# Kernel optimization log

Hardware: AMD Instinct MI355X
Metric: run time of the kernel (lower is better)

The kernel has to match this reference:

```python
import jax, jax.numpy as jnp
import numpy as np

B, DZ, H, DY = 4096, 512, 2048, 10
N_STEPS = 64
SCALE = 0.02  # matches param_ulow/uhigh magnitude


def setup_inputs() -> dict:
    key = jax.random.key(0)
    ks = jax.random.split(key, 6)
    x = jax.random.normal(ks[0], (B, DZ), dtype=jnp.float32)
    A = jax.random.normal(ks[1], (DZ, DZ), dtype=jnp.float32) * SCALE
    W1 = jax.random.normal(ks[2], (H, DZ), dtype=jnp.float32) * SCALE
    b1 = jax.random.normal(ks[3], (H,), dtype=jnp.float32) * SCALE
    W2 = jax.random.normal(ks[4], (DY, H), dtype=jnp.float32) * SCALE
    b2 = jax.random.normal(ks[5], (DY,), dtype=jnp.float32) * SCALE
    return {"x": x, "A": A, "W1": W1, "b1": b1, "W2": W2, "b2": b2,
            "n_steps": N_STEPS}


def reference(x, A, W1, b1, W2, b2, n_steps):
    # Z0 = P @ x with P = I  => Z0 = x
    # dz/dt = einsum('ji,bi->bj', A, z) = z @ A.T ; explicit Euler on [0, 1]
    dt = jnp.float32(1.0 / n_steps)

    def euler_step(z, _):
        return z + dt * (z @ A.T), None

    zT, _ = jax.lax.scan(euler_step, x, None, length=n_steps)  # [B, DZ]
    # Q MLP (n_layers=3): Linear -> ReLU -> Linear
    h = jax.nn.relu(zT @ W1.T + b1)  # [B, H]
    y = h @ W2.T + b2                # [B, DY]
    return y
```

## Files before the change

kernel.cpp:

```cpp
#include <hip/hip_runtime.h>
#include <hip/hip_bf16.h>

#define B_SZ 4096
#define DZ   512
#define H_SZ 2048
#define DY   10

#define C2 0.4921875f
#define C3 0.158935546875f
#define C4 0.037872314453125f
#define C5 ((float)(7624512.0/1073741824.0))
#define C6 ((float)(74974368.0/68719476736.0))

typedef __attribute__((ext_vector_type(8))) __bf16 bf16x8;
typedef __attribute__((ext_vector_type(4))) float  f32x4;
typedef __attribute__((ext_vector_type(8))) unsigned short us8;

__device__ inline unsigned short f2bf(float f) {
    unsigned u = __float_as_uint(f);
    u += 0x7fffu + ((u >> 16) & 1u);
    return (unsigned short)(u >> 16);
}
__device__ inline float bf2f(unsigned short s) {
    return __uint_as_float(((unsigned)s) << 16);
}

union SqSmem {
    struct { unsigned short A[64 * 64]; unsigned short B[64 * 64]; } s;
    float epi[64 * 68];
};

#define MFMA_STEP(acc)                                                        \
    {                                                                         \
        _Pragma("unroll")                                                     \
        for (int ks = 0; ks < 2; ++ks) {                                      \
            bf16x8 af[2], bfr[2];                                             \
            _Pragma("unroll")                                                 \
            for (int i = 0; i < 2; ++i) {                                     \
                int ra = wm + i * 16 + l16, ca = (ks * 4 + quad) ^ (ra & 7);  \
                af[i] = *(const bf16x8*)&sm.s.A[ra * 64 + ca * 8];            \
                int rb = wn + i * 16 + l16, cb = (ks * 4 + quad) ^ (rb & 7);  \
                bfr[i] = *(const bf16x8*)&sm.s.B[rb * 64 + cb * 8];           \
            }                                                                 \
            _Pragma("unroll")                                                 \
            for (int i = 0; i < 2; ++i)                                       \
                _Pragma("unroll")                                             \
                for (int j = 0; j < 2; ++j)                                   \
                    acc[i][j] = __builtin_amdgcn_mfma_f32_16x16x32_bf16(      \
                        af[i], bfr[j], acc[i][j], 0, 0, 0);                   \
        }                                                                     \
    }

#define ACC_TO_EPI(acc)                                                       \
    {                                                                         \
        _Pragma("unroll")                                                     \
        for (int i = 0; i < 2; ++i)                                           \
            _Pragma("unroll")                                                 \
            for (int j = 0; j < 2; ++j)                                       \
                _Pragma("unroll")                                             \
                for (int rr = 0; rr < 4; ++rr)                                \
                    sm.epi[(wm + i * 16 + quad * 4 + rr) * 68 +               \
                           wn + j * 16 + l16] = acc[i][j][rr];                \
        __syncthreads();                                                      \
    }

__device__ inline void gemm64_mfma(const unsigned short* __restrict__ Arows,
                                   const unsigned short* __restrict__ Brows,
                                   int m0, int n0, int t, SqSmem& sm) {
    const int lane = t & 63, w = t >> 6, quad = lane >> 4, l16 = lane & 15;
    const int wm = (w & 1) * 32, wn = (w >> 1) * 32;
    f32x4 acc[2][2];
#pragma unroll
    for (int i = 0; i < 2; ++i)
#pragma unroll
        for (int j = 0; j < 2; ++j) acc[i][j] = (f32x4){0.f, 0.f, 0.f, 0.f};
    for (int kt = 0; kt < 8; ++kt) {
#pragma unroll
        for (int c = 0; c < 2; ++c) {
            int idx = c * 256 + t, row = idx >> 3, cc = idx & 7;
            int ccs = cc ^ (row & 7);
            *(us8*)&sm.s.A[row * 64 + ccs * 8] =
                *(const us8*)&Arows[(size_t)(m0 + row) * 512 + kt * 64 + cc * 8];
            *(us8*)&sm.s.B[row * 64 + ccs * 8] =
                *(const us8*)&Brows[(size_t)(n0 + row) * 512 + kt * 64 + cc * 8];
        }
        __syncthreads();
        MFMA_STEP(acc)
        __syncthreads();
    }
    ACC_TO_EPI(acc)
}

__device__ inline void gemm64_f32src(const float* __restrict__ Arows,
                                     const float* __restrict__ Bsrc,
                                     int m0, int n0, int t, SqSmem& sm) {
    const int lane = t & 63, w = t >> 6, quad = lane >> 4, l16 = lane & 15;
    const int wm = (w & 1) * 32, wn = (w >> 1) * 32;
    const int r = t >> 2, cq = t & 3;
    f32x4 acc[2][2];
#pragma unroll
    for (int i = 0; i < 2; ++i)
#pragma unroll
        for (int j = 0; j < 2; ++j) acc[i][j] = (f32x4){0.f, 0.f, 0.f, 0.f};
    for (int kt = 0; kt < 8; ++kt) {
        float va[16];
#pragma unroll
        for (int u = 0; u < 4; ++u) {
            float4 f = *(const float4*)&Arows[(size_t)(m0 + r) * 512 + kt * 64 + cq * 16 + u * 4];
            va[u * 4 + 0] = f.x; va[u * 4 + 1] = f.y;
            va[u * 4 + 2] = f.z; va[u * 4 + 3] = f.w;
        }
#pragma unroll
        for (int j2 = 0; j2 < 2; ++j2) {
            us8 h;
#pragma unroll
            for (int j = 0; j < 8; ++j) h[j] = f2bf(va[j2 * 8 + j]);
            int cc = cq * 2 + j2;
            *(us8*)&sm.s.A[r * 64 + (cc ^ (r & 7)) * 8] = h;
        }
#pragma unroll
        for (int u = 0; u < 4; ++u) {
            float4 f = *(const float4*)&Bsrc[(size_t)(kt * 64 + r) * 512 + n0 + cq * 16 + u * 4];
            float vv[4] = {f.x, f.y, f.z, f.w};
#pragma unroll
            for (int j = 0; j < 4; ++j) {
                int n = cq * 16 + u * 4 + j;
                sm.s.B[n * 64 + ((r >> 3) ^ (n & 7)) * 8 + (r & 7)] = f2bf(vv[j]);
            }
        }
        __syncthreads();
        MFMA_STEP(acc)
        __syncthreads();
    }
    ACC_TO_EPI(acc)
}

__device__ inline void epi_out_bf(unsigned short* __restrict__ dst, int m0,
                                  int n0, int t, SqSmem& sm) {
    const int r = t >> 2, cq = t & 3;
    us8 h0, h1;
#pragma unroll
    for (int j = 0; j < 8; ++j) {
        h0[j] = f2bf(sm.epi[r * 68 + cq * 16 + j]);
        h1[j] = f2bf(sm.epi[r * 68 + cq * 16 + 8 + j]);
    }
    *(us8*)&dst[(size_t)(m0 + r) * 512 + n0 + cq * 16]     = h0;
    *(us8*)&dst[(size_t)(m0 + r) * 512 + n0 + cq * 16 + 8] = h1;
}
__device__ inline void epi_out_bfT(unsigned short* __restrict__ dst, int m0,
                                   int n0, int t, SqSmem& sm) {
    const int cf = t >> 2, rq = t & 3;
    us8 o0, o1;
#pragma unroll
    for (int i = 0; i < 8; ++i) {
        o0[i] = f2bf(sm.epi[(rq * 16 + i) * 68 + cf]);
        o1[i] = f2bf(sm.epi[(rq * 16 + 8 + i) * 68 + cf]);
    }
    *(us8*)&dst[(size_t)(n0 + cf) * 512 + m0 + rq * 16]     = o0;
    *(us8*)&dst[(size_t)(n0 + cf) * 512 + m0 + rq * 16 + 8] = o1;
}

__global__ __launch_bounds__(256) void k_s1(
    const float* __restrict__ A, const float* __restrict__ x,
    const float* __restrict__ W1, const float* __restrict__ b2,
    unsigned short* __restrict__ A2_bf, unsigned short* __restrict__ A2T_bf,
    unsigned short* __restrict__ AT_bf, unsigned short* __restrict__ U1_bf,
    unsigned short* __restrict__ x_bf, float* __restrict__ y) {
    __shared__ SqSmem sm;
    const int b = blockIdx.x, t = threadIdx.x;
    const int gid = b * 256 + t;

    const float4* x4 = (const float4*)x;
#pragma unroll
    for (int i = 0; i < 3; ++i) {
        int id = gid + i * 98304;
        if (id < 262144) {
            float4 v0 = x4[(size_t)id * 2], v1 = x4[(size_t)id * 2 + 1];
            us8 o;
            o[0] = f2bf(v0.x); o[1] = f2bf(v0.y); o[2] = f2bf(v0.z); o[3] = f2bf(v0.w);
            o[4] = f2bf(v1.x); o[5] = f2bf(v1.y); o[6] = f2bf(v1.z); o[7] = f2bf(v1.w);
            *(us8*)&x_bf[(size_t)id * 8] = o;
        }
    }
    if (gid < B_SZ * DY) y[gid] = b2[gid % 10];

    if (b < 64) {
        const int m0 = (b >> 3) * 64, n0 = (b & 7) * 64;
        gemm64_f32src(A, A, m0, n0, t, sm);
        epi_out_bf(A2_bf, m0, n0, t, sm);
        epi_out_bfT(A2T_bf, m0, n0, t, sm);
    } else if (b < 128) {
        const int bb = b - 64, m0 = (bb >> 3) * 64, n0 = (bb & 7) * 64;
        const int r = t >> 2, cq = t & 3;
#pragma unroll
        for (int u = 0; u < 4; ++u) {
            float4 f = *(const float4*)&A[(size_t)(m0 + r) * 512 + n0 + cq * 16 + u * 4];
            sm.epi[r * 68 + cq * 16 + u * 4 + 0] = f.x;
            sm.epi[r * 68 + cq * 16 + u * 4 + 1] = f.y;
            sm.epi[r * 68 + cq * 16 + u * 4 + 2] = f.z;
            sm.epi[r * 68 + cq * 16 + u * 4 + 3] = f.w;
        }
        __syncthreads();
        epi_out_bfT(AT_bf, m0, n0, t, sm);
    } else {
        const int bb = b - 128, m0 = (bb >> 3) * 64, n0 = (bb & 7) * 64;
        gemm64_f32src(W1, A, m0, n0, t, sm);
        epi_out_bf(U1_bf, m0, n0, t, sm);
    }
}

__global__ __launch_bounds__(256) void k_s2(
    const unsigned short* __restrict__ A2_bf,
    const unsigned short* __restrict__ A2T_bf,
    const unsigned short* __restrict__ AT_bf,
    const unsigned short* __restrict__ U1_bf,
    unsigned short* __restrict__ A3T_bf, unsigned short* __restrict__ U2_bf,
    unsigned short* __restrict__ U3_bf) {
    __shared__ SqSmem sm;
    const int b = blockIdx.x, t = threadIdx.x;
    if (b < 64) {
        const int m0 = (b >> 3) * 64, n0 = (b & 7) * 64;
        gemm64_mfma(A2_bf, AT_bf, m0, n0, t, sm);
        epi_out_bfT(A3T_bf, m0, n0, t, sm);
    } else if (b < 320) {
        const int bb = b - 64, m0 = (bb >> 3) * 64, n0 = (bb & 7) * 64;
        gemm64_mfma(U1_bf, AT_bf, m0, n0, t, sm);
        epi_out_bf(U2_bf, m0, n0, t, sm);
    } else {
        const int bb = b - 320, m0 = (bb >> 3) * 64, n0 = (bb & 7) * 64;
        gemm64_mfma(U1_bf, A2T_bf, m0, n0, t, sm);
        epi_out_bf(U3_bf, m0, n0, t, sm);
    }
}

__global__ __launch_bounds__(256) void k_s3(
    const float* __restrict__ W1, const unsigned short* __restrict__ U1_bf,
    const unsigned short* __restrict__ U2_bf,
    const unsigned short* __restrict__ U3_bf,
    const unsigned short* __restrict__ A3T_bf,
    unsigned short* __restrict__ w1f) {
    __shared__ SqSmem sm;
    const int b = blockIdx.x, t = threadIdx.x;
    const int m0 = (b >> 3) * 64, n0 = (b & 7) * 64;
    const int lane = t & 63, w = t >> 6, quad = lane >> 4, l16 = lane & 15;
    const int wm = (w & 1) * 32, wn = (w >> 1) * 32;
    f32x4 acc[2][2];
#pragma unroll
    for (int i = 0; i < 2; ++i)
#pragma unroll
        for (int j = 0; j < 2; ++j) acc[i][j] = (f32x4){0.f, 0.f, 0.f, 0.f};
    for (int kt = 0; kt < 8; ++kt) {
#pragma unroll
        for (int c = 0; c < 2; ++c) {
            int idx = c * 256 + t, row = idx >> 3, cc = idx & 7;
            int ccs = cc ^ (row & 7);
            size_t ga = (size_t)(m0 + row) * 512 + kt * 64 + cc * 8;
            us8 u1 = *(const us8*)&U1_bf[ga];
            us8 u2 = *(const us8*)&U2_bf[ga];
            us8 u3 = *(const us8*)&U3_bf[ga];
            us8 g;
#pragma unroll
            for (int j = 0; j < 8; ++j)
                g[j] = f2bf(C4 * bf2f(u1[j]) + C5 * bf2f(u2[j]) + C6 * bf2f(u3[j]));
            *(us8*)&sm.s.A[row * 64 + ccs * 8] = g;
            *(us8*)&sm.s.B[row * 64 + ccs * 8] =
                *(const us8*)&A3T_bf[(size_t)(n0 + row) * 512 + kt * 64 + cc * 8];
        }
        __syncthreads();
        MFMA_STEP(acc)
        __syncthreads();
    }
    ACC_TO_EPI(acc)
    const int r = t >> 2, cq = t & 3;
    size_t gbase = (size_t)(m0 + r) * 512 + n0 + cq * 16;
    us8 u1a = *(const us8*)&U1_bf[gbase], u1b = *(const us8*)&U1_bf[gbase + 8];
    us8 u2a = *(const us8*)&U2_bf[gbase], u2b = *(const us8*)&U2_bf[gbase + 8];
    us8 u3a = *(const us8*)&U3_bf[gbase], u3b = *(const us8*)&U3_bf[gbase + 8];
    us8 h0, h1;
#pragma unroll
    for (int u = 0; u < 2; ++u) {
        float4 wv = *(const float4*)&W1[gbase + u * 4];
        float4 wv2 = *(const float4*)&W1[gbase + 8 + u * 4];
#pragma unroll
        for (int j = 0; j < 4; ++j) {
            int e = u * 4 + j;
            float wj = (j == 0 ? wv.x : j == 1 ? wv.y : j == 2 ? wv.z : wv.w);
            float wj2 = (j == 0 ? wv2.x : j == 1 ? wv2.y : j == 2 ? wv2.z : wv2.w);
            h0[e] = f2bf(wj + bf2f(u1a[e]) + C2 * bf2f(u2a[e]) +
                         C3 * bf2f(u3a[e]) + sm.epi[r * 68 + cq * 16 + e]);
            h1[e] = f2bf(wj2 + bf2f(u1b[e]) + C2 * bf2f(u2b[e]) +
                         C3 * bf2f(u3b[e]) + sm.epi[r * 68 + cq * 16 + 8 + e]);
        }
    }
    *(us8*)&w1f[gbase]     = h0;
    *(us8*)&w1f[gbase + 8] = h1;
}

union SmemU {
    struct { unsigned short A[128 * 64]; unsigned short B[128 * 64]; } s;
    struct { unsigned short h[128 * 130]; float w2[DY * 132]; } e;
};

__global__ __launch_bounds__(256, 2) void mlp_kernel(
    const unsigned short* __restrict__ x_bf,
    const unsigned short* __restrict__ w1f,
    const float* __restrict__ b1, const float* __restrict__ W2,
    float* __restrict__ y) {
    __shared__ SmemU sm;
    const int t    = threadIdx.x;
    const int lane = t & 63, w = t >> 6;
    const int quad = lane >> 4, l16 = lane & 15;
    const int wm = (w & 1) * 64, wn = (w >> 1) * 64;
    const int m0g = blockIdx.x * 128, n0g = blockIdx.y * 128;

    f32x4 acc[4][4];
#pragma unroll
    for (int i = 0; i < 4; ++i)
#pragma unroll
        for (int j = 0; j < 4; ++j) acc[i][j] = (f32x4){0.f, 0.f, 0.f, 0.f};

    for (int kt = 0; kt < 8; ++kt) {
#pragma unroll
        for (int c = 0; c < 4; ++c) {
            int idx = c * 256 + t;
            int row = idx >> 3, cc = idx & 7;
            int ccs = cc ^ (row & 7);
            us8 va = *(const us8*)&x_bf[(size_t)(m0g + row) * 512 + kt * 64 + cc * 8];
            *(us8*)&sm.s.A[row * 64 + ccs * 8] = va;
            us8 vb = *(const us8*)&w1f[(size_t)(n0g + row) * 512 + kt * 64 + cc * 8];
            *(us8*)&sm.s.B[row * 64 + ccs * 8] = vb;
        }
        __syncthreads();
#pragma unroll
        for (int ks = 0; ks < 2; ++ks) {
            bf16x8 af[4], bfr[4];
#pragma unroll
            for (int i = 0; i < 4; ++i) {
                int ra = wm + i * 16 + l16;
                int rb = wn + i * 16 + l16;
                int ca = (ks * 4 + quad) ^ (ra & 7);
                int cb = (ks * 4 + quad) ^ (rb & 7);
                af[i]  = *(const bf16x8*)&sm.s.A[ra * 64 + ca * 8];
                bfr[i] = *(const bf16x8*)&sm.s.B[rb * 64 + cb * 8];
            }
#pragma unroll
            for (int i = 0; i < 4; ++i)
#pragma unroll
                for (int j = 0; j < 4; ++j)
                    acc[i][j] = __builtin_amdgcn_mfma_f32_16x16x32_bf16(
                        af[i], bfr[j], acc[i][j], 0, 0, 0);
        }
        __syncthreads();
    }

    float bias[4];
#pragma unroll
    for (int j = 0; j < 4; ++j) bias[j] = b1[n0g + wn + j * 16 + l16];
#pragma unroll
    for (int i = 0; i < 4; ++i)
#pragma unroll
        for (int j = 0; j < 4; ++j)
#pragma unroll
            for (int r = 0; r < 4; ++r) {
                float h = acc[i][j][r] + bias[j];
                h = h > 0.f ? h : 0.f;
                sm.e.h[(wn + j * 16 + l16) * 130 + (wm + i * 16 + quad * 4 + r)] = f2bf(h);
            }
    for (int i = t; i < DY * 128; i += 256) {
        int d = i >> 7, n = i & 127;
        sm.e.w2[d * 132 + n] = W2[(size_t)d * H_SZ + n0g + n];
    }
    __syncthreads();
    {
        int m = t >> 1, dg = t & 1;
        float s0 = 0.f, s1 = 0.f, s2 = 0.f, s3 = 0.f, s4 = 0.f;
        const float* wrow = &sm.e.w2[dg * 5 * 132];
#pragma unroll 4
        for (int n = 0; n < 128; ++n) {
            float h = bf2f(sm.e.h[n * 130 + m]);
            s0 += h * wrow[n];
            s1 += h * wrow[132 + n];
            s2 += h * wrow[264 + n];
            s3 += h * wrow[396 + n];
            s4 += h * wrow[528 + n];
        }
        float* yp = &y[(size_t)(m0g + m) * DY + dg * 5];
        atomicAdd(yp + 0, s0);
        atomicAdd(yp + 1, s1);
        atomicAdd(yp + 2, s2);
        atomicAdd(yp + 3, s3);
        atomicAdd(yp + 4, s4);
    }
}

extern "C" void kernel_launch(void* const* d_in, const int* in_sizes, int n_in,
                              void* d_out, int out_size, void* d_ws, size_t ws_size,
                              hipStream_t stream) {
    const float* x  = (const float*)d_in[0];
    const float* A  = (const float*)d_in[1];
    const float* W1 = (const float*)d_in[2];
    const float* b1 = (const float*)d_in[3];
    const float* W2 = (const float*)d_in[4];
    const float* b2 = (const float*)d_in[5];
    float* y = (float*)d_out;

    char* ws = (char*)d_ws;
    const size_t HMB = 512u * 1024, MB = 1u << 20;
    unsigned short* AT_bf  = (unsigned short*)(ws);
    unsigned short* A2_bf  = (unsigned short*)(ws + 1 * HMB);
    unsigned short* A2T_bf = (unsigned short*)(ws + 2 * HMB);
    unsigned short* A3T_bf = (unsigned short*)(ws + 3 * HMB);
    unsigned short* U1_bf  = (unsigned short*)(ws + 2 * MB);
    unsigned short* U2_bf  = (unsigned short*)(ws + 4 * MB);
    unsigned short* U3_bf  = (unsigned short*)(ws + 6 * MB);
    unsigned short* w1f    = (unsigned short*)(ws + 8 * MB);
    unsigned short* x_bf   = (unsigned short*)(ws + 10 * MB);

    k_s1<<<384, 256, 0, stream>>>(A, x, W1, b2, A2_bf, A2T_bf, AT_bf, U1_bf,
                                  x_bf, y);
    k_s2<<<576, 256, 0, stream>>>(A2_bf, A2T_bf, AT_bf, U1_bf, A3T_bf, U2_bf,
                                  U3_bf);
    k_s3<<<256, 256, 0, stream>>>(W1, U1_bf, U2_bf, U3_bf, A3T_bf, w1f);
    mlp_kernel<<<dim3(32, 16), dim3(256), 0, stream>>>(x_bf, w1f, b1, W2, y);
}
```

Baseline: 166.9 us.

## Split fp32 conversion into its own pass and use bf16 MFMA GEMMs for first stage

```diff
diff --git a/kernel.cpp b/kernel.cpp
--- a/kernel.cpp
+++ b/kernel.cpp
@@ -91,50 +91,6 @@
     ACC_TO_EPI(acc)
 }
 
-__device__ inline void gemm64_f32src(const float* __restrict__ Arows,
-                                     const float* __restrict__ Bsrc,
-                                     int m0, int n0, int t, SqSmem& sm) {
-    const int lane = t & 63, w = t >> 6, quad = lane >> 4, l16 = lane & 15;
-    const int wm = (w & 1) * 32, wn = (w >> 1) * 32;
-    const int r = t >> 2, cq = t & 3;
-    f32x4 acc[2][2];
-#pragma unroll
-    for (int i = 0; i < 2; ++i)
-#pragma unroll
-        for (int j = 0; j < 2; ++j) acc[i][j] = (f32x4){0.f, 0.f, 0.f, 0.f};
-    for (int kt = 0; kt < 8; ++kt) {
-        float va[16];
-#pragma unroll
-        for (int u = 0; u < 4; ++u) {
-            float4 f = *(const float4*)&Arows[(size_t)(m0 + r) * 512 + kt * 64 + cq * 16 + u * 4];
-            va[u * 4 + 0] = f.x; va[u * 4 + 1] = f.y;
-            va[u * 4 + 2] = f.z; va[u * 4 + 3] = f.w;
-        }
-#pragma unroll
-        for (int j2 = 0; j2 < 2; ++j2) {
-            us8 h;
-#pragma unroll
-            for (int j = 0; j < 8; ++j) h[j] = f2bf(va[j2 * 8 + j]);
-            int cc = cq * 2 + j2;
-            *(us8*)&sm.s.A[r * 64 + (cc ^ (r & 7)) * 8] = h;
-        }
-#pragma unroll
-        for (int u = 0; u < 4; ++u) {
-            float4 f = *(const float4*)&Bsrc[(size_t)(kt * 64 + r) * 512 + n0 + cq * 16 + u * 4];
-            float vv[4] = {f.x, f.y, f.z, f.w};
-#pragma unroll
-            for (int j = 0; j < 4; ++j) {
-                int n = cq * 16 + u * 4 + j;
-                sm.s.B[n * 64 + ((r >> 3) ^ (n & 7)) * 8 + (r & 7)] = f2bf(vv[j]);
-            }
-        }
-        __syncthreads();
-        MFMA_STEP(acc)
-        __syncthreads();
-    }
-    ACC_TO_EPI(acc)
-}
-
 __device__ inline void epi_out_bf(unsigned short* __restrict__ dst, int m0,
                                   int n0, int t, SqSmem& sm) {
     const int r = t >> 2, cq = t & 3;
@@ -160,56 +116,80 @@
     *(us8*)&dst[(size_t)(n0 + cf) * 512 + m0 + rq * 16 + 8] = o1;
 }
 
-__global__ __launch_bounds__(256) void k_s1(
+__global__ __launch_bounds__(256) void k_conv(
     const float* __restrict__ A, const float* __restrict__ x,
     const float* __restrict__ W1, const float* __restrict__ b2,
-    unsigned short* __restrict__ A2_bf, unsigned short* __restrict__ A2T_bf,
-    unsigned short* __restrict__ AT_bf, unsigned short* __restrict__ U1_bf,
-    unsigned short* __restrict__ x_bf, float* __restrict__ y) {
+    unsigned short* __restrict__ A_bf, unsigned short* __restrict__ AT_bf,
+    unsigned short* __restrict__ x_bf, unsigned short* __restrict__ w1_bf,
+    float* __restrict__ y) {
     __shared__ SqSmem sm;
     const int b = blockIdx.x, t = threadIdx.x;
-    const int gid = b * 256 + t;
 
     const float4* x4 = (const float4*)x;
 #pragma unroll
-    for (int i = 0; i < 3; ++i) {
-        int id = gid + i * 98304;
-        if (id < 262144) {
-            float4 v0 = x4[(size_t)id * 2], v1 = x4[(size_t)id * 2 + 1];
-            us8 o;
-            o[0] = f2bf(v0.x); o[1] = f2bf(v0.y); o[2] = f2bf(v0.z); o[3] = f2bf(v0.w);
-            o[4] = f2bf(v1.x); o[5] = f2bf(v1.y); o[6] = f2bf(v1.z); o[7] = f2bf(v1.w);
-            *(us8*)&x_bf[(size_t)id * 8] = o;
-        }
-    }
-    if (gid < B_SZ * DY) y[gid] = b2[gid % 10];
+    for (int i = 0; i < 4; ++i) {
+        int id = b * 1024 + i * 256 + t;
+        float4 v0 = x4[(size_t)id * 2], v1 = x4[(size_t)id * 2 + 1];
+        us8 o;
+        o[0] = f2bf(v0.x); o[1] = f2bf(v0.y); o[2] = f2bf(v0.z); o[3] = f2bf(v0.w);
+        o[4] = f2bf(v1.x); o[5] = f2bf(v1.y); o[6] = f2bf(v1.z); o[7] = f2bf(v1.w);
+        *(us8*)&x_bf[(size_t)id * 8] = o;
+    }
+    const float4* w4 = (const float4*)W1;
+#pragma unroll
+    for (int i = 0; i < 2; ++i) {
+        int id = b * 512 + i * 256 + t;
+        float4 v0 = w4[(size_t)id * 2], v1 = w4[(size_t)id * 2 + 1];
+        us8 o;
+        o[0] = f2bf(v0.x); o[1] = f2bf(v0.y); o[2] = f2bf(v0.z); o[3] = f2bf(v0.w);
+        o[4] = f2bf(v1.x); o[5] = f2bf(v1.y); o[6] = f2bf(v1.z); o[7] = f2bf(v1.w);
+        *(us8*)&w1_bf[(size_t)id * 8] = o;
+    }
+    if (t < 160) { int id = b * 160 + t; y[id] = b2[id % 10]; }
 
     if (b < 64) {
         const int m0 = (b >> 3) * 64, n0 = (b & 7) * 64;
-        gemm64_f32src(A, A, m0, n0, t, sm);
+        const int r = t >> 2, cq = t & 3;
+        float vals[16];
+#pragma unroll
+        for (int u = 0; u < 4; ++u) {
+            float4 f = *(const float4*)&A[(size_t)(m0 + r) * 512 + n0 + cq * 16 + u * 4];
+            vals[u * 4 + 0] = f.x; vals[u * 4 + 1] = f.y;
+            vals[u * 4 + 2] = f.z; vals[u * 4 + 3] = f.w;
+        }
+        us8 h0, h1;
+#pragma unroll
+        for (int j = 0; j < 8; ++j) { h0[j] = f2bf(vals[j]); h1[j] = f2bf(vals[8 + j]); }
+        *(us8*)&A_bf[(size_t)(m0 + r) * 512 + n0 + cq * 16]     = h0;
+        *(us8*)&A_bf[(size_t)(m0 + r) * 512 + n0 + cq * 16 + 8] = h1;
+#pragma unroll
+        for (int j = 0; j < 16; ++j) sm.epi[r * 68 + cq * 16 + j] = vals[j];
+        __syncthreads();
+        epi_out_bfT(AT_bf, m0, n0, t, sm);
+    }
+}
+
+__global__ __launch_bounds__(256) void k_g1(
+    const unsigned short* __restrict__ A_bf,
+    const unsigned short* __restrict__ AT_bf,
+    const unsigned short* __restrict__ w1_bf,
+    unsigned short* __restrict__ A2_bf, unsigned short* __restrict__ A2T_bf,
+    unsigned short* __restrict__ U1_bf) {
+    __shared__ SqSmem sm;
+    const int b = blockIdx.x, t = threadIdx.x;
+    if (b < 64) {
+        const int m0 = (b >> 3) * 64, n0 = (b & 7) * 64;
+        gemm64_mfma(A_bf, AT_bf, m0, n0, t, sm);
         epi_out_bf(A2_bf, m0, n0, t, sm);
         epi_out_bfT(A2T_bf, m0, n0, t, sm);
-    } else if (b < 128) {
+    } else {
         const int bb = b - 64, m0 = (bb >> 3) * 64, n0 = (bb & 7) * 64;
-        const int r = t >> 2, cq = t & 3;
-#pragma unroll
-        for (int u = 0; u < 4; ++u) {
-            float4 f = *(const float4*)&A[(size_t)(m0 + r) * 512 + n0 + cq * 16 + u * 4];
-            sm.epi[r * 68 + cq * 16 + u * 4 + 0] = f.x;
-            sm.epi[r * 68 + cq * 16 + u * 4 + 1] = f.y;
-            sm.epi[r * 68 + cq * 16 + u * 4 + 2] = f.z;
-            sm.epi[r * 68 + cq * 16 + u * 4 + 3] = f.w;
-        }
-        __syncthreads();
-        epi_out_bfT(AT_bf, m0, n0, t, sm);
-    } else {
-        const int bb = b - 128, m0 = (bb >> 3) * 64, n0 = (bb & 7) * 64;
-        gemm64_f32src(W1, A, m0, n0, t, sm);
+        gemm64_mfma(w1_bf, AT_bf, m0, n0, t, sm);
         epi_out_bf(U1_bf, m0, n0, t, sm);
     }
 }
 
-__global__ __launch_bounds__(256) void k_s2(
+__global__ __launch_bounds__(256) void k_g2(
     const unsigned short* __restrict__ A2_bf,
     const unsigned short* __restrict__ A2T_bf,
     const unsigned short* __restrict__ AT_bf,
@@ -233,7 +213,7 @@
     }
 }
 
-__global__ __launch_bounds__(256) void k_s3(
+__global__ __launch_bounds__(256) void k_g3(
     const float* __restrict__ W1, const unsigned short* __restrict__ U1_bf,
     const unsigned short* __restrict__ U2_bf,
     const unsigned short* __restrict__ U3_bf,
@@ -301,7 +281,7 @@
     struct { unsigned short h[128 * 130]; float w2[DY * 132]; } e;
 };
 
-__global__ __launch_bounds__(256, 2) void mlp_kernel(
+__global__ __launch_bounds__(256, 3) void mlp_kernel(
     const unsigned short* __restrict__ x_bf,
     const unsigned short* __restrict__ w1f,
     const float* __restrict__ b1, const float* __restrict__ W2,
@@ -406,20 +386,22 @@
 
     char* ws = (char*)d_ws;
     const size_t HMB = 512u * 1024, MB = 1u << 20;
-    unsigned short* AT_bf  = (unsigned short*)(ws);
-    unsigned short* A2_bf  = (unsigned short*)(ws + 1 * HMB);
-    unsigned short* A2T_bf = (unsigned short*)(ws + 2 * HMB);
-    unsigned short* A3T_bf = (unsigned short*)(ws + 3 * HMB);
-    unsigned short* U1_bf  = (unsigned short*)(ws + 2 * MB);
-    unsigned short* U2_bf  = (unsigned short*)(ws + 4 * MB);
-    unsigned short* U3_bf  = (unsigned short*)(ws + 6 * MB);
-    unsigned short* w1f    = (unsigned short*)(ws + 8 * MB);
-    unsigned short* x_bf   = (unsigned short*)(ws + 10 * MB);
-
-    k_s1<<<384, 256, 0, stream>>>(A, x, W1, b2, A2_bf, A2T_bf, AT_bf, U1_bf,
-                                  x_bf, y);
-    k_s2<<<576, 256, 0, stream>>>(A2_bf, A2T_bf, AT_bf, U1_bf, A3T_bf, U2_bf,
+    unsigned short* A_bf   = (unsigned short*)(ws);
+    unsigned short* AT_bf  = (unsigned short*)(ws + 1 * HMB);
+    unsigned short* A2_bf  = (unsigned short*)(ws + 2 * HMB);
+    unsigned short* A2T_bf = (unsigned short*)(ws + 3 * HMB);
+    unsigned short* A3T_bf = (unsigned short*)(ws + 4 * HMB);
+    unsigned short* U1_bf  = (unsigned short*)(ws + 3 * MB);
+    unsigned short* U2_bf  = (unsigned short*)(ws + 5 * MB);
+    unsigned short* U3_bf  = (unsigned short*)(ws + 7 * MB);
+    unsigned short* w1_bf  = (unsigned short*)(ws + 9 * MB);
+    unsigned short* w1f    = (unsigned short*)(ws + 11 * MB);
+    unsigned short* x_bf   = (unsigned short*)(ws + 13 * MB);
+
+    k_conv<<<256, 256, 0, stream>>>(A, x, W1, b2, A_bf, AT_bf, x_bf, w1_bf, y);
+    k_g1<<<320, 256, 0, stream>>>(A_bf, AT_bf, w1_bf, A2_bf, A2T_bf, U1_bf);
+    k_g2<<<576, 256, 0, stream>>>(A2_bf, A2T_bf, AT_bf, U1_bf, A3T_bf, U2_bf,
                                   U3_bf);
-    k_s3<<<256, 256, 0, stream>>>(W1, U1_bf, U2_bf, U3_bf, A3T_bf, w1f);
+    k_g3<<<256, 256, 0, stream>>>(W1, U1_bf, U2_bf, U3_bf, A3T_bf, w1f);
     mlp_kernel<<<dim3(32, 16), dim3(256), 0, stream>>>(x_bf, w1f, b1, W2, y);
 }
```

Result: slower. 171.5 us (+2.7%).

## Fuse x fp32-to-bf16 conversion into MLP GEMM and halve its N tile

Applied to the files above, without the earlier changes.

```diff
diff --git a/kernel.cpp b/kernel.cpp
--- a/kernel.cpp
+++ b/kernel.cpp
@@ -160,28 +160,15 @@
     *(us8*)&dst[(size_t)(n0 + cf) * 512 + m0 + rq * 16 + 8] = o1;
 }
 
-__global__ __launch_bounds__(256) void k_s1(
-    const float* __restrict__ A, const float* __restrict__ x,
-    const float* __restrict__ W1, const float* __restrict__ b2,
+__global__ __launch_bounds__(256) void k_g1(
+    const float* __restrict__ A, const float* __restrict__ W1,
+    const float* __restrict__ b2,
     unsigned short* __restrict__ A2_bf, unsigned short* __restrict__ A2T_bf,
     unsigned short* __restrict__ AT_bf, unsigned short* __restrict__ U1_bf,
-    unsigned short* __restrict__ x_bf, float* __restrict__ y) {
+    float* __restrict__ y) {
     __shared__ SqSmem sm;
     const int b = blockIdx.x, t = threadIdx.x;
     const int gid = b * 256 + t;
-
-    const float4* x4 = (const float4*)x;
-#pragma unroll
-    for (int i = 0; i < 3; ++i) {
-        int id = gid + i * 98304;
-        if (id < 262144) {
-            float4 v0 = x4[(size_t)id * 2], v1 = x4[(size_t)id * 2 + 1];
-            us8 o;
-            o[0] = f2bf(v0.x); o[1] = f2bf(v0.y); o[2] = f2bf(v0.z); o[3] = f2bf(v0.w);
-            o[4] = f2bf(v1.x); o[5] = f2bf(v1.y); o[6] = f2bf(v1.z); o[7] = f2bf(v1.w);
-            *(us8*)&x_bf[(size_t)id * 8] = o;
-        }
-    }
     if (gid < B_SZ * DY) y[gid] = b2[gid % 10];
 
     if (b < 64) {
@@ -209,7 +196,7 @@
     }
 }
 
-__global__ __launch_bounds__(256) void k_s2(
+__global__ __launch_bounds__(256) void k_g2(
     const unsigned short* __restrict__ A2_bf,
     const unsigned short* __restrict__ A2T_bf,
     const unsigned short* __restrict__ AT_bf,
@@ -233,7 +220,7 @@
     }
 }
 
-__global__ __launch_bounds__(256) void k_s3(
+__global__ __launch_bounds__(256) void k_g3(
     const float* __restrict__ W1, const unsigned short* __restrict__ U1_bf,
     const unsigned short* __restrict__ U2_bf,
     const unsigned short* __restrict__ U3_bf,
@@ -297,12 +284,12 @@
 }
 
 union SmemU {
-    struct { unsigned short A[128 * 64]; unsigned short B[128 * 64]; } s;
-    struct { unsigned short h[128 * 130]; float w2[DY * 132]; } e;
+    struct { unsigned short A[128 * 64]; unsigned short B[64 * 64]; } s;
+    struct { unsigned short h[64 * 130]; float w2[DY * 68]; } e;
 };
 
-__global__ __launch_bounds__(256, 2) void mlp_kernel(
-    const unsigned short* __restrict__ x_bf,
+__global__ __launch_bounds__(256) void mlp_kernel(
+    const float* __restrict__ x,
     const unsigned short* __restrict__ w1f,
     const float* __restrict__ b1, const float* __restrict__ W2,
     float* __restrict__ y) {
@@ -310,79 +297,89 @@
     const int t    = threadIdx.x;
     const int lane = t & 63, w = t >> 6;
     const int quad = lane >> 4, l16 = lane & 15;
-    const int wm = (w & 1) * 64, wn = (w >> 1) * 64;
-    const int m0g = blockIdx.x * 128, n0g = blockIdx.y * 128;
-
-    f32x4 acc[4][4];
+    const int wm = (w >> 1) * 64, wn = (w & 1) * 32;
+    const int m0g = blockIdx.x * 128, n0g = blockIdx.y * 64;
+
+    f32x4 acc[4][2];
 #pragma unroll
     for (int i = 0; i < 4; ++i)
 #pragma unroll
-        for (int j = 0; j < 4; ++j) acc[i][j] = (f32x4){0.f, 0.f, 0.f, 0.f};
+        for (int j = 0; j < 2; ++j) acc[i][j] = (f32x4){0.f, 0.f, 0.f, 0.f};
 
     for (int kt = 0; kt < 8; ++kt) {
 #pragma unroll
         for (int c = 0; c < 4; ++c) {
-            int idx = c * 256 + t;
-            int row = idx >> 3, cc = idx & 7;
+            int idx = c * 256 + t, row = idx >> 3, cc = idx & 7;
             int ccs = cc ^ (row & 7);
-            us8 va = *(const us8*)&x_bf[(size_t)(m0g + row) * 512 + kt * 64 + cc * 8];
-            *(us8*)&sm.s.A[row * 64 + ccs * 8] = va;
-            us8 vb = *(const us8*)&w1f[(size_t)(n0g + row) * 512 + kt * 64 + cc * 8];
-            *(us8*)&sm.s.B[row * 64 + ccs * 8] = vb;
+            const float* gp = &x[(size_t)(m0g + row) * 512 + kt * 64 + cc * 8];
+            float4 f0 = *(const float4*)gp;
+            float4 f1 = *(const float4*)(gp + 4);
+            us8 o;
+            o[0] = f2bf(f0.x); o[1] = f2bf(f0.y); o[2] = f2bf(f0.z); o[3] = f2bf(f0.w);
+            o[4] = f2bf(f1.x); o[5] = f2bf(f1.y); o[6] = f2bf(f1.z); o[7] = f2bf(f1.w);
+            *(us8*)&sm.s.A[row * 64 + ccs * 8] = o;
+        }
+#pragma unroll
+        for (int c = 0; c < 2; ++c) {
+            int idx = c * 256 + t, row = idx >> 3, cc = idx & 7;
+            int ccs = cc ^ (row & 7);
+            *(us8*)&sm.s.B[row * 64 + ccs * 8] =
+                *(const us8*)&w1f[(size_t)(n0g + row) * 512 + kt * 64 + cc * 8];
         }
         __syncthreads();
 #pragma unroll
         for (int ks = 0; ks < 2; ++ks) {
-            bf16x8 af[4], bfr[4];
+            bf16x8 af[4], bfr[2];
 #pragma unroll
             for (int i = 0; i < 4; ++i) {
-                int ra = wm + i * 16 + l16;
-                int rb = wn + i * 16 + l16;
-                int ca = (ks * 4 + quad) ^ (ra & 7);
-                int cb = (ks * 4 + quad) ^ (rb & 7);
-                af[i]  = *(const bf16x8*)&sm.s.A[ra * 64 + ca * 8];
-                bfr[i] = *(const bf16x8*)&sm.s.B[rb * 64 + cb * 8];
+                int ra = wm + i * 16 + l16, ca = (ks * 4 + quad) ^ (ra & 7);
+                af[i] = *(const bf16x8*)&sm.s.A[ra * 64 + ca * 8];
             }
 #pragma unroll
+            for (int j = 0; j < 2; ++j) {
+                int rb = wn + j * 16 + l16, cb = (ks * 4 + quad) ^ (rb & 7);
+                bfr[j] = *(const bf16x8*)&sm.s.B[rb * 64 + cb * 8];
+            }
+#pragma unroll
             for (int i = 0; i < 4; ++i)
 #pragma unroll
-                for (int j = 0; j < 4; ++j)
+                for (int j = 0; j < 2; ++j)
                     acc[i][j] = __builtin_amdgcn_mfma_f32_16x16x32_bf16(
                         af[i], bfr[j], acc[i][j], 0, 0, 0);
         }
         __syncthreads();
     }
 
-    float bias[4];
-#pragma unroll
-    for (int j = 0; j < 4; ++j) bias[j] = b1[n0g + wn + j * 16 + l16];
+    float bias[2];
+#pragma unroll
+    for (int j = 0; j < 2; ++j) bias[j] = b1[n0g + wn + j * 16 + l16];
 #pragma unroll
     for (int i = 0; i < 4; ++i)
 #pragma unroll
-        for (int j = 0; j < 4; ++j)
+        for (int j = 0; j < 2; ++j)
 #pragma unroll
             for (int r = 0; r < 4; ++r) {
                 float h = acc[i][j][r] + bias[j];
                 h = h > 0.f ? h : 0.f;
                 sm.e.h[(wn + j * 16 + l16) * 130 + (wm + i * 16 + quad * 4 + r)] = f2bf(h);
             }
-    for (int i = t; i < DY * 128; i += 256) {
-        int d = i >> 7, n = i & 127;
-        sm.e.w2[d * 132 + n] = W2[(size_t)d * H_SZ + n0g + n];
+    for (int i = t; i < DY * 64; i += 256) {
+        int d = i >> 6, n = i & 63;
+        sm.e.w2[d * 68 + n] = W2[(size_t)d * H_SZ + n0g + n];
     }
     __syncthreads();
     {
         int m = t >> 1, dg = t & 1;
         float s0 = 0.f, s1 = 0.f, s2 = 0.f, s3 = 0.f, s4 = 0.f;
-        const float* wrow = &sm.e.w2[dg * 5 * 132];
+        const float* wrow = &sm.e.w2[dg * 5 * 68];
 #pragma unroll 4
-        for (int n = 0; n < 128; ++n) {
+        for (int n = 0; n < 64; ++n) {
             float h = bf2f(sm.e.h[n * 130 + m]);
             s0 += h * wrow[n];
-            s1 += h * wrow[132 + n];
-            s2 += h * wrow[264 + n];
-            s3 += h * wrow[396 + n];
-            s4 += h * wrow[528 + n];
+            s1 += h * wrow[68 + n];
+            s2 += h * wrow[136 + n];
+            s3 += h * wrow[204 + n];
+            s4 += h * wrow[272 + n];
         }
         float* yp = &y[(size_t)(m0g + m) * DY + dg * 5];
         atomicAdd(yp + 0, s0);
@@ -414,12 +411,10 @@
     unsigned short* U2_bf  = (unsigned short*)(ws + 4 * MB);
     unsigned short* U3_bf  = (unsigned short*)(ws + 6 * MB);
     unsigned short* w1f    = (unsigned short*)(ws + 8 * MB);
-    unsigned short* x_bf   = (unsigned short*)(ws + 10 * MB);
-
-    k_s1<<<384, 256, 0, stream>>>(A, x, W1, b2, A2_bf, A2T_bf, AT_bf, U1_bf,
-                                  x_bf, y);
-    k_s2<<<576, 256, 0, stream>>>(A2_bf, A2T_bf, AT_bf, U1_bf, A3T_bf, U2_bf,
+
+    k_g1<<<384, 256, 0, stream>>>(A, W1, b2, A2_bf, A2T_bf, AT_bf, U1_bf, y);
+    k_g2<<<576, 256, 0, stream>>>(A2_bf, A2T_bf, AT_bf, U1_bf, A3T_bf, U2_bf,
                                   U3_bf);
-    k_s3<<<256, 256, 0, stream>>>(W1, U1_bf, U2_bf, U3_bf, A3T_bf, w1f);
-    mlp_kernel<<<dim3(32, 16), dim3(256), 0, stream>>>(x_bf, w1f, b1, W2, y);
-}
+    k_g3<<<256, 256, 0, stream>>>(W1, U1_bf, U2_bf, U3_bf, A3T_bf, w1f);
+    mlp_kernel<<<dim3(32, 32), dim3(256), 0, stream>>>(x, w1f, b1, W2, y);
+}
```

Measured after the change: 180.3 us. 1.08x slower.
